# Optimization experiments

Measured on AMD Instinct MI355X. Metric: run time of the kernel, lower is better.

## Reference

```python
import jax, jax.numpy as jnp
import numpy as np

N = 100000   # nodes
E = 1600000  # edges
IN, H, C = 128, 128, 40


def setup_inputs() -> dict:
    key = jax.random.key(0)
    ks = jax.random.split(key, 8)
    feat = jax.random.normal(ks[0], (N, IN), jnp.float32)
    src = jax.random.randint(ks[1], (E,), 0, N, jnp.int32)
    dst = jax.random.randint(ks[2], (E,), 0, N, jnp.int32)
    # Glorot-ish init like dgl GraphConv.reset_parameters
    W0 = jax.random.normal(ks[3], (IN, H), jnp.float32) * (1.0 / np.sqrt(IN))
    W1 = jax.random.normal(ks[4], (H, H), jnp.float32) * (1.0 / np.sqrt(H))
    W2 = jax.random.normal(ks[5], (H, C), jnp.float32) * (1.0 / np.sqrt(H))
    b0 = jnp.zeros((H,), jnp.float32)
    b1 = jnp.zeros((H,), jnp.float32)
    b2 = jnp.zeros((C,), jnp.float32)
    return {"feat": feat, "src": src, "dst": dst,
            "W0": W0, "b0": b0, "W1": W1, "b1": b1, "W2": W2, "b2": b2}


def _graph_conv(h, src, dst, W, b):
    # dgl GraphConv with norm='both': D_out^{-1/2} pre-scale, sum-aggregate,
    # D_in^{-1/2} post-scale; degrees clamped to min 1. Weight applied before
    # aggregation (in_feats >= out_feats path) -- math is identical either way.
    ones = jnp.ones((src.shape[0],), h.dtype)
    deg_out = jnp.maximum(jax.ops.segment_sum(ones, src, num_segments=N), 1.0)
    deg_in = jnp.maximum(jax.ops.segment_sum(ones, dst, num_segments=N), 1.0)
    h = h * (deg_out ** -0.5)[:, None]
    h = h @ W                                   # [N, out]
    agg = jax.ops.segment_sum(h[src], dst, num_segments=N)  # gather+scatter
    return agg * (deg_in ** -0.5)[:, None] + b


def reference(feat, src, dst, W0, b0, W1, b1, W2, b2):
    h = jax.nn.relu(_graph_conv(feat, src, dst, W0, b0))  # dropout p=0 -> identity
    h = jax.nn.relu(_graph_conv(h, src, dst, W1, b1))
    return _graph_conv(h, src, dst, W2, b2)
```

## Files before the change

kernel.cpp:

```cpp
#include <hip/hip_runtime.h>

#define NN 100000
#define EE 1600000
#define ELLW 64
#define GEMMN ((NN + 31) / 32)
#define BQ ((EE / 4 + 511) / 512)
#define GRID_BG (BQ * 5)

#define NBKT 196
#define BSH 9
#define CAPD 10240
#define CAPS 10240

typedef int iv4 __attribute__((ext_vector_type(4)));

__device__ __forceinline__ unsigned int pack_bf2(float a, float b) {
    unsigned int ua = __float_as_uint(a);
    ua += 0x7FFFu + ((ua >> 16) & 1u);
    unsigned int ub = __float_as_uint(b);
    ub += 0x7FFFu + ((ub >> 16) & 1u);
    return (ua >> 16) | (ub & 0xFFFF0000u);
}

__device__ __forceinline__ unsigned short bf1(float a) {
    unsigned int ua = __float_as_uint(a);
    ua += 0x7FFFu + ((ua >> 16) & 1u);
    return (unsigned short)(ua >> 16);
}

__device__ __forceinline__ void gemm128_body(const float* __restrict__ X,
                                             const float* __restrict__ W, unsigned int* __restrict__ Y,
                                             int row0, int tid, float* Xs) {
    const float4* X4 = (const float4*)X;
#pragma unroll
    for (int idx = tid; idx < 1024; idx += 256) {
        int r = idx & 31, c4 = idx >> 5;
        int row = row0 + r;
        float4 v = X4[(size_t)row * 32 + c4];
        Xs[(c4 * 4 + 0) * 32 + r] = v.x;
        Xs[(c4 * 4 + 1) * 32 + r] = v.y;
        Xs[(c4 * 4 + 2) * 32 + r] = v.z;
        Xs[(c4 * 4 + 3) * 32 + r] = v.w;
    }
    __syncthreads();
    int cg = tid & 31;
    int rg = tid >> 5;
    float a[4][4];
#pragma unroll
    for (int r = 0; r < 4; ++r)
#pragma unroll
        for (int c = 0; c < 4; ++c) a[r][c] = 0.f;
    const float4* W4 = (const float4*)W;
#pragma unroll 4
    for (int k = 0; k < 128; ++k) {
        float4 xv = *(const float4*)&Xs[k * 32 + rg * 4];
        float4 wv = W4[k * 32 + cg];
        float xr[4] = {xv.x, xv.y, xv.z, xv.w};
        float wc[4] = {wv.x, wv.y, wv.z, wv.w};
#pragma unroll
        for (int r = 0; r < 4; ++r)
#pragma unroll
            for (int c = 0; c < 4; ++c) a[r][c] = fmaf(xr[r], wc[c], a[r][c]);
    }
    int rbase = row0 + rg * 4;
    uint2* Y2 = (uint2*)Y;
#pragma unroll
    for (int r = 0; r < 4; ++r) {
        Y2[(size_t)(rbase + r) * 32 + cg] =
            make_uint2(pack_bf2(a[r][0], a[r][1]), pack_bf2(a[r][2], a[r][3]));
    }
}

__global__ __launch_bounds__(256) void k_buildA_gemm0(const int* __restrict__ src, const int* __restrict__ dst,
                                                      int* __restrict__ curD, int* __restrict__ curS,
                                                      unsigned int* __restrict__ stagD,
                                                      unsigned short* __restrict__ stagS,
                                                      const float* __restrict__ X, const float* __restrict__ W,
                                                      unsigned int* __restrict__ Y) {
    __shared__ float Xs[128 * 32];
    int tid = threadIdx.x;
    int q = blockIdx.x / 5, rem = blockIdx.x % 5;
    if (rem) {
        int g = q * 4 + (rem - 1);
        if (g < GEMMN) gemm128_body(X, W, Y, g * 32, tid, Xs);
        return;
    }
    int* sh = (int*)Xs;
    for (int i = tid; i < 1536; i += 256) sh[i] = 0;
    __syncthreads();

    const iv4* s4p = (const iv4*)src;
    const iv4* d4p = (const iv4*)dst;
    const int n4 = EE / 4;
    iv4 sv[2], dv[2];
    int have[2];
#pragma unroll
    for (int h = 0; h < 2; ++h) {
        int i4 = q * 512 + h * 256 + tid;
        have[h] = (i4 < n4);
        if (have[h]) {
            sv[h] = __builtin_nontemporal_load(&s4p[i4]);
            dv[h] = __builtin_nontemporal_load(&d4p[i4]);
        }
    }
#pragma unroll
    for (int h = 0; h < 2; ++h) {
        if (have[h]) {
            int ss[4] = {sv[h].x, sv[h].y, sv[h].z, sv[h].w};
            int dd[4] = {dv[h].x, dv[h].y, dv[h].z, dv[h].w};
#pragma unroll
            for (int k = 0; k < 4; ++k) {
                atomicAdd(&sh[dd[k] >> BSH], 1);
                atomicAdd(&sh[256 + (ss[k] >> BSH)], 1);
            }
        }
    }
    __syncthreads();
    if (tid < NBKT) {
        int hd = sh[tid];
        sh[512 + tid] = hd ? atomicAdd(&curD[tid], hd) : 0;
        int hs = sh[256 + tid];
        sh[768 + tid] = hs ? atomicAdd(&curS[tid], hs) : 0;
    }
    __syncthreads();
#pragma unroll
    for (int h = 0; h < 2; ++h) {
        if (have[h]) {
            int ss[4] = {sv[h].x, sv[h].y, sv[h].z, sv[h].w};
            int dd[4] = {dv[h].x, dv[h].y, dv[h].z, dv[h].w};
#pragma unroll
            for (int k = 0; k < 4; ++k) {
                int bd = dd[k] >> BSH;
                int od = atomicAdd(&sh[1024 + bd], 1);
                stagD[(size_t)bd * CAPD + sh[512 + bd] + od] =
                    ((unsigned int)ss[k] << BSH) | (unsigned int)(dd[k] & 511);
                int bs = ss[k] >> BSH;
                int os = atomicAdd(&sh[1280 + bs], 1);
                stagS[(size_t)bs * CAPS + sh[768 + bs] + os] = (unsigned short)(ss[k] & 511);
            }
        }
    }
}

__global__ __launch_bounds__(256) void k_buildB(const int* __restrict__ curD, const int* __restrict__ curS,
                                                const unsigned int* __restrict__ stagD,
                                                const unsigned short* __restrict__ stagS,
                                                int* __restrict__ din, int* __restrict__ dout,
                                                int* __restrict__ ell) {
    __shared__ int cl[512];
    int tid = threadIdx.x;
    int b = blockIdx.x;
    for (int i = tid; i < 512; i += 256) cl[i] = 0;
    __syncthreads();
    if (b < NBKT) {
        int n0 = b << BSH;
        int cnt = min(curD[b], CAPD);
        const unsigned int* sg = stagD + (size_t)b * CAPD;
        for (int i = tid; i < cnt; i += 256) {
            unsigned int v = sg[i];
            int dlow = (int)(v & 511u);
            int s = (int)(v >> BSH);
            int p = atomicAdd(&cl[dlow], 1);
            if (p < ELLW) ell[(size_t)(n0 + dlow) * ELLW + p] = s;
        }
        __syncthreads();
        for (int i = tid; i < 512; i += 256) {
            int node = n0 + i;
            if (node < NN) din[node] = cl[i];
        }
    } else {
        int bs = b - NBKT;
        int n0 = bs << BSH;
        int cnt = min(curS[bs], CAPS);
        const unsigned short* sg = stagS + (size_t)bs * CAPS;
        for (int i = tid; i < cnt; i += 256) {
            atomicAdd(&cl[sg[i]], 1);
        }
        __syncthreads();
        for (int i = tid; i < 512; i += 256) {
            int node = n0 + i;
            if (node < NN) dout[node] = cl[i];
        }
    }
}

#define GG_BATCH(CL, SC, JB, CNT, SO) do {                                         \
    int cc_[8]; float mk_[8]; uint2 t_[8];                                         \
    _Pragma("unroll")                                                              \
    for (int k = 0; k < 8; ++k) {                                                  \
        int slot = (JB) + k;                                                       \
        int srcl = (hl << 5) | (slot & 31);                                        \
        cc_[k] = __shfl((CL), srcl);                                               \
        float sw = (SO) ? __shfl((SC), srcl) : 1.f;                                \
        mk_[k] = (slot < (CNT)) ? sw : 0.f;                                        \
    }                                                                              \
    _Pragma("unroll")                                                              \
    for (int k = 0; k < 8; ++k) {                                                  \
        t_[k] = make_uint2(0u, 0u);                                                \
        if ((JB) + k < (CNT)) t_[k] = h2v[(size_t)cc_[k] * 32 + ln];               \
    }                                                                              \
    _Pragma("unroll")                                                              \
    for (int k = 0; k < 8; ++k) {                                                  \
        a0 = fmaf(mk_[k], __uint_as_float(t_[k].x << 16), a0);                     \
        a1 = fmaf(mk_[k], __uint_as_float(t_[k].x & 0xFFFF0000u), a1);             \
        a2 = fmaf(mk_[k], __uint_as_float(t_[k].y << 16), a2);                     \
        a3 = fmaf(mk_[k], __uint_as_float(t_[k].y & 0xFFFF0000u), a3);             \
    }                                                                              \
} while (0)

__global__ __launch_bounds__(256) void k_gathergemm128(const unsigned int* __restrict__ h,
                                                       const int* __restrict__ din, const int* __restrict__ dout,
                                                       const int* __restrict__ ell,
                                                       const float* __restrict__ bias,
                                                       const float* __restrict__ W,
                                                       unsigned int* __restrict__ Y, int so_mode) {
    __shared__ float Xs[128 * 36];
    int tid = threadIdx.x;
    int wv = tid >> 6, lane = tid & 63;
    int hl = lane >> 5, ln = lane & 31;
    int row0 = blockIdx.x * 32;
    int nb = row0 + wv * 8 + hl;
    int dvh[4], dvo[4], cl0[4], cl1[4];
    float sc0[4], sc1[4];
#pragma unroll
    for (int it = 0; it < 4; ++it) {
        int v = nb + it * 2;
        dvh[it] = din[v];
        dvo[it] = dout[v];
        cl0[it] = ell[(size_t)v * ELLW + ln];
        cl1[it] = ell[(size_t)v * ELLW + 32 + ln];
    }
#pragma unroll
    for (int it = 0; it < 4; ++it) {
        int cnt = min(dvh[it], ELLW);
        int d0 = 1, d1 = 1;
        if (so_mode && ln < cnt) d0 = dout[cl0[it]];
        if (so_mode && ln + 32 < cnt) d1 = dout[cl1[it]];
        sc0[it] = rsqrtf((float)max(1, d0));
        sc1[it] = rsqrtf((float)max(1, d1));
    }
    float4 bb = ((const float4*)bias)[ln];
    const uint2* h2v = (const uint2*)h;
#pragma unroll
    for (int it = 0; it < 4; ++it) {
        int r = wv * 8 + it * 2 + hl;
        int cnt = min(dvh[it], ELLW);
        float a0 = 0.f, a1 = 0.f, a2 = 0.f, a3 = 0.f;
        for (int jb = 0; jb < 32; jb += 8) {
            if (!__any(jb < cnt)) break;
            GG_BATCH(cl0[it], sc0[it], jb, cnt, so_mode);
        }
        if (__any(cnt > 32)) {
            for (int jb = 32; jb < 64; jb += 8) {
                if (!__any(jb < cnt)) break;
                GG_BATCH(cl1[it], sc1[it], jb, cnt, so_mode);
            }
        }
        float si = rsqrtf((float)max(1, dvh[it]));
        float so = rsqrtf((float)max(1, dvo[it]));
        Xs[(4 * ln + 0) * 36 + r] = fmaxf(a0 * si + bb.x, 0.f) * so;
        Xs[(4 * ln + 1) * 36 + r] = fmaxf(a1 * si + bb.y, 0.f) * so;
        Xs[(4 * ln + 2) * 36 + r] = fmaxf(a2 * si + bb.z, 0.f) * so;
        Xs[(4 * ln + 3) * 36 + r] = fmaxf(a3 * si + bb.w, 0.f) * so;
    }
    __syncthreads();
    int cg = tid & 31, rg = tid >> 5;
    float a[4][4];
#pragma unroll
    for (int r = 0; r < 4; ++r)
#pragma unroll
        for (int c = 0; c < 4; ++c) a[r][c] = 0.f;
    const float4* W4 = (const float4*)W;
#pragma unroll 4
    for (int k = 0; k < 128; ++k) {
        float4 xv = *(const float4*)&Xs[k * 36 + rg * 4];
        float4 wv4 = W4[k * 32 + cg];
        float xr[4] = {xv.x, xv.y, xv.z, xv.w};
        float wc[4] = {wv4.x, wv4.y, wv4.z, wv4.w};
#pragma unroll
        for (int r = 0; r < 4; ++r)
#pragma unroll
            for (int c = 0; c < 4; ++c) a[r][c] = fmaf(xr[r], wc[c], a[r][c]);
    }
    int rbase = row0 + rg * 4;
    uint2* Y2 = (uint2*)Y;
#pragma unroll
    for (int r = 0; r < 4; ++r) {
        Y2[(size_t)(rbase + r) * 32 + cg] =
            make_uint2(pack_bf2(a[r][0], a[r][1]), pack_bf2(a[r][2], a[r][3]));
    }
}

__global__ __launch_bounds__(256) void k_gathergemm40(const unsigned int* __restrict__ h,
                                                      const int* __restrict__ din, const int* __restrict__ dout,
                                                      const int* __restrict__ ell,
                                                      const float* __restrict__ bias,
                                                      const float* __restrict__ W,
                                                      unsigned short* __restrict__ Y) {
    __shared__ float Xs[128 * 36];
    int tid = threadIdx.x;
    int wv = tid >> 6, lane = tid & 63;
    int hl = lane >> 5, ln = lane & 31;
    int row0 = blockIdx.x * 32;
    int nb = row0 + wv * 8 + hl;
    int dvh[4], dvo[4], cl0[4], cl1[4];
#pragma unroll
    for (int it = 0; it < 4; ++it) {
        int v = nb + it * 2;
        dvh[it] = din[v];
        dvo[it] = dout[v];
        cl0[it] = ell[(size_t)v * ELLW + ln];
        cl1[it] = ell[(size_t)v * ELLW + 32 + ln];
    }
    float4 bb = ((const float4*)bias)[ln];
    const uint2* h2v = (const uint2*)h;
#pragma unroll
    for (int it = 0; it < 4; ++it) {
        int r = wv * 8 + it * 2 + hl;
        int cnt = min(dvh[it], ELLW);
        float a0 = 0.f, a1 = 0.f, a2 = 0.f, a3 = 0.f;
        float dummy = 0.f;
        for (int jb = 0; jb < 32; jb += 8) {
            if (!__any(jb < cnt)) break;
            GG_BATCH(cl0[it], dummy, jb, cnt, 0);
        }
        if (__any(cnt > 32)) {
            for (int jb = 32; jb < 64; jb += 8) {
                if (!__any(jb < cnt)) break;
                GG_BATCH(cl1[it], dummy, jb, cnt, 0);
            }
        }
        float si = rsqrtf((float)max(1, dvh[it]));
        float so = rsqrtf((float)max(1, dvo[it]));
        Xs[(4 * ln + 0) * 36 + r] = fmaxf(a0 * si + bb.x, 0.f) * so;
        Xs[(4 * ln + 1) * 36 + r] = fmaxf(a1 * si + bb.y, 0.f) * so;
        Xs[(4 * ln + 2) * 36 + r] = fmaxf(a2 * si + bb.z, 0.f) * so;
        Xs[(4 * ln + 3) * 36 + r] = fmaxf(a3 * si + bb.w, 0.f) * so;
    }
    __syncthreads();
    int rg = tid >> 3;
    int cg = tid & 7;
    float a[5] = {0.f, 0.f, 0.f, 0.f, 0.f};
#pragma unroll 4
    for (int k = 0; k < 128; ++k) {
        float x = Xs[k * 36 + rg];
#pragma unroll
        for (int c = 0; c < 5; ++c) a[c] = fmaf(x, W[k * 40 + cg * 5 + c], a[c]);
    }
    size_t yb = (size_t)(row0 + rg) * 64 + cg * 5;
#pragma unroll
    for (int c = 0; c < 5; ++c) Y[yb + c] = bf1(a[c]);
}

__global__ __launch_bounds__(256) void k_gather40(const unsigned int* __restrict__ h, const int* __restrict__ din,
                                                  const int* __restrict__ ell,
                                                  const float* __restrict__ b, float* __restrict__ out, int n) {
    int tid = threadIdx.x;
    int wv = tid >> 6, lane = tid & 63;
    int hl = lane >> 5, ln = lane & 31;
    int v = blockIdx.x * 8 + wv * 2 + hl;
    int dv = din[v];
    int cnt = min(dv, ELLW);
    int cl0 = ell[(size_t)v * ELLW + ln];
    int cl1 = ell[(size_t)v * ELLW + 32 + ln];
    float s0 = 0.f, s1 = 0.f;
    for (int half = 0; half < 2; ++half) {
        int clh = half ? cl1 : cl0;
        int jb0 = half * 32;
        if (half && !__any(cnt > 32)) break;
        for (int jb = jb0; jb < jb0 + 32; jb += 8) {
            if (!__any(jb < cnt)) break;
            int cc_[8]; float mk_[8]; unsigned int t_[8];
#pragma unroll
            for (int k = 0; k < 8; ++k) {
                int slot = jb + k;
                int srcl = (hl << 5) | (slot & 31);
                cc_[k] = __shfl(clh, srcl);
                mk_[k] = (slot < cnt) ? 1.f : 0.f;
            }
#pragma unroll
            for (int k = 0; k < 8; ++k) {
                t_[k] = 0u;
                if (jb + k < cnt) t_[k] = h[(size_t)cc_[k] * 32 + ln];
            }
#pragma unroll
            for (int k = 0; k < 8; ++k) {
                s0 = fmaf(mk_[k], __uint_as_float(t_[k] << 16), s0);
                s1 = fmaf(mk_[k], __uint_as_float(t_[k] & 0xFFFF0000u), s1);
            }
        }
    }
    if (ln < 20) {
        float si = rsqrtf((float)max(1, dv));
        float2 bb = ((const float2*)b)[ln];
        ((float2*)out)[(size_t)v * 20 + ln] = make_float2(s0 * si + bb.x, s1 * si + bb.y);
    }
}

extern "C" void kernel_launch(void* const* d_in, const int* in_sizes, int n_in,
                              void* d_out, int out_size, void* d_ws, size_t ws_size,
                              hipStream_t stream) {
    const float* feat = (const float*)d_in[0];
    const int*   src  = (const int*)d_in[1];
    const int*   dst  = (const int*)d_in[2];
    const float* W0   = (const float*)d_in[3];
    const float* b0   = (const float*)d_in[4];
    const float* W1   = (const float*)d_in[5];
    const float* b1   = (const float*)d_in[6];
    const float* W2   = (const float*)d_in[7];
    const float* b2   = (const float*)d_in[8];
    float* out = (float*)d_out;

    char* w = (char*)d_ws;
    int*   din       = (int*)w;    w += (size_t)NN * 4;
    int*   dout      = (int*)w;    w += (size_t)NN * 4;
    int*   curD      = (int*)w;    w += 256 * 4;
    int*   curS      = (int*)w;    w += 256 * 4;
    int*   ell       = (int*)w;    w += (size_t)NN * ELLW * 4;
    unsigned int*   stagD = (unsigned int*)w;   w += (size_t)NBKT * CAPD * 4;
    unsigned short* stagS = (unsigned short*)w; w += (size_t)NBKT * CAPS * 2;
    unsigned int* h2 = (unsigned int*)w; w += (size_t)NN * 128 * 2;
    unsigned int* h2b = (unsigned int*)w; w += (size_t)NN * 128 * 2;
    unsigned int* h40 = (unsigned int*)w; w += (size_t)NN * 32 * 4;

    (void)hipMemsetAsync(d_ws, 0, (size_t)NN * 8 + 2048, stream);

    k_buildA_gemm0<<<GRID_BG, 256, 0, stream>>>(src, dst, curD, curS, stagD, stagS, feat, W0, h2);
    k_buildB<<<NBKT * 2, 256, 0, stream>>>(curD, curS, stagD, stagS, din, dout, ell);
    k_gathergemm128<<<GEMMN, 256, 0, stream>>>(h2, din, dout, ell, b0, W1, h2b, 1);
    k_gathergemm40<<<GEMMN, 256, 0, stream>>>(h2b, din, dout, ell, b1, W2, (unsigned short*)h40);
    k_gather40<<<NN / 8, 256, 0, stream>>>(h40, din, ell, b2, out, NN);
}
```

Baseline: 477.2 us.

## Split fused gather-GEMM by feature half with XCC-aware work queue and combine pass

Splits each fused gather+GEMM layer into two work items per 32-row tile, one per half of the input features. Each item gathers only 64 columns and computes a partial GEMM into fp32 scratch, and a separate combine kernel sums the two partials and packs them to bf16. Work items come from an atomic queue keyed by the XCC id so that each feature half tends to stay on the same set of dies, aiming to improve L2 locality for the gathered rows. This adds fp32 partial writes and reads plus two extra launches, falls back to the old path when the workspace is too small, and also skips loading the second ELL half when the degree is at most 32.

```diff
diff --git a/kernel.cpp b/kernel.cpp
--- a/kernel.cpp
+++ b/kernel.cpp
@@ -12,7 +12,10 @@
 #define CAPD 10240
 #define CAPS 10240
 
+#define XCC_GETREG_IMM 63508
+
 typedef int iv4 __attribute__((ext_vector_type(4)));
+typedef float fv4 __attribute__((ext_vector_type(4)));
 
 __device__ __forceinline__ unsigned int pack_bf2(float a, float b) {
     unsigned int ua = __float_as_uint(a);
@@ -35,16 +38,14 @@
 #pragma unroll
     for (int idx = tid; idx < 1024; idx += 256) {
         int r = idx & 31, c4 = idx >> 5;
-        int row = row0 + r;
-        float4 v = X4[(size_t)row * 32 + c4];
+        float4 v = X4[(size_t)(row0 + r) * 32 + c4];
         Xs[(c4 * 4 + 0) * 32 + r] = v.x;
         Xs[(c4 * 4 + 1) * 32 + r] = v.y;
         Xs[(c4 * 4 + 2) * 32 + r] = v.z;
         Xs[(c4 * 4 + 3) * 32 + r] = v.w;
     }
     __syncthreads();
-    int cg = tid & 31;
-    int rg = tid >> 5;
+    int cg = tid & 31, rg = tid >> 5;
     float a[4][4];
 #pragma unroll
     for (int r = 0; r < 4; ++r)
@@ -181,6 +182,218 @@
             int node = n0 + i;
             if (node < NN) dout[node] = cl[i];
         }
+    }
+}
+
+#define GH_BATCH(CL, SC, JB, CNT) do {                                             \
+    int cc_[8]; float mk_[8]; unsigned int t_[8];                                  \
+    _Pragma("unroll")                                                              \
+    for (int k = 0; k < 8; ++k) {                                                  \
+        int slot = (JB) + k;                                                       \
+        int srcl = (hl << 5) | (slot & 31);                                        \
+        cc_[k] = __shfl((CL), srcl);                                               \
+        float sw = so_mode ? __shfl((SC), srcl) : 1.f;                             \
+        mk_[k] = (slot < (CNT)) ? sw : 0.f;                                        \
+    }                                                                              \
+    _Pragma("unroll")                                                              \
+    for (int k = 0; k < 8; ++k) {                                                  \
+        t_[k] = 0u;                                                                \
+        if ((JB) + k < (CNT)) t_[k] = hh[(size_t)cc_[k] * 64 + ln];                \
+    }                                                                              \
+    _Pragma("unroll")                                                              \
+    for (int k = 0; k < 8; ++k) {                                                  \
+        a0 = fmaf(mk_[k], __uint_as_float(t_[k] << 16), a0);                       \
+        a1 = fmaf(mk_[k], __uint_as_float(t_[k] & 0xFFFF0000u), a1);               \
+    }                                                                              \
+} while (0)
+
+__device__ __forceinline__ int grab_item(int* q, int tid, int* sh_item) {
+    if (tid == 0) {
+        unsigned int xcc = __builtin_amdgcn_s_getreg(XCC_GETREG_IMM);
+        int g = (xcc >> 2) & 1;
+        int t = atomicAdd(&q[g], 1);
+        if (t >= GEMMN) { g ^= 1; t = atomicAdd(&q[g], 1); }
+        *sh_item = (t < GEMMN) ? (t * 2 + g) : -1;
+    }
+    __syncthreads();
+    return *sh_item;
+}
+
+__global__ __launch_bounds__(256) void k_gg128half(const unsigned int* __restrict__ h,
+                                                   const int* __restrict__ din, const int* __restrict__ dout,
+                                                   const int* __restrict__ ell,
+                                                   const float* __restrict__ bias,
+                                                   const float* __restrict__ W,
+                                                   float* __restrict__ P, int* __restrict__ q,
+                                                   int so_mode) {
+    __shared__ float Xs[64 * 36];
+    __shared__ int sh_item;
+    int tid = threadIdx.x;
+    int item = grab_item(q, tid, &sh_item);
+    if (item < 0) return;
+    int tile = item >> 1, half = item & 1;
+    int wv = tid >> 6, lane = tid & 63, hl = lane >> 5, ln = lane & 31;
+    int row0 = tile * 32;
+    int nb = row0 + wv * 8 + hl;
+    int dvh[4], dvo[4], cl0[4], cl1[4];
+    float sc0[4], sc1[4];
+#pragma unroll
+    for (int it = 0; it < 4; ++it) {
+        int v = nb + it * 2;
+        dvh[it] = din[v];
+        dvo[it] = dout[v];
+        cl0[it] = ell[(size_t)v * ELLW + ln];
+        cl1[it] = (dvh[it] > 32) ? ell[(size_t)v * ELLW + 32 + ln] : 0;
+    }
+#pragma unroll
+    for (int it = 0; it < 4; ++it) {
+        int cnt = min(dvh[it], ELLW);
+        int d0 = 1, d1 = 1;
+        if (so_mode && ln < cnt) d0 = dout[cl0[it]];
+        if (so_mode && ln + 32 < cnt) d1 = dout[cl1[it]];
+        sc0[it] = rsqrtf((float)max(1, d0));
+        sc1[it] = rsqrtf((float)max(1, d1));
+    }
+    float2 bb = ((const float2*)bias)[32 * half + ln];
+    const unsigned int* hh = h + 32 * half;
+#pragma unroll
+    for (int it = 0; it < 4; ++it) {
+        int r = wv * 8 + it * 2 + hl;
+        int cnt = min(dvh[it], ELLW);
+        float a0 = 0.f, a1 = 0.f;
+        for (int jb = 0; jb < 32; jb += 8) {
+            if (!__any(jb < cnt)) break;
+            GH_BATCH(cl0[it], sc0[it], jb, cnt);
+        }
+        if (__any(cnt > 32)) {
+            for (int jb = 32; jb < 64; jb += 8) {
+                if (!__any(jb < cnt)) break;
+                GH_BATCH(cl1[it], sc1[it], jb, cnt);
+            }
+        }
+        float si = rsqrtf((float)max(1, dvh[it]));
+        float so = rsqrtf((float)max(1, dvo[it]));
+        Xs[(2 * ln + 0) * 36 + r] = fmaxf(a0 * si + bb.x, 0.f) * so;
+        Xs[(2 * ln + 1) * 36 + r] = fmaxf(a1 * si + bb.y, 0.f) * so;
+    }
+    __syncthreads();
+    int cg = tid & 31, rg = tid >> 5;
+    float a[4][4];
+#pragma unroll
+    for (int r = 0; r < 4; ++r)
+#pragma unroll
+        for (int c = 0; c < 4; ++c) a[r][c] = 0.f;
+    const float4* W4 = (const float4*)W;
+    int kbase = 64 * half;
+#pragma unroll 4
+    for (int k = 0; k < 64; ++k) {
+        float4 xv = *(const float4*)&Xs[k * 36 + rg * 4];
+        float4 wv4 = W4[(kbase + k) * 32 + cg];
+        float xr[4] = {xv.x, xv.y, xv.z, xv.w};
+        float wc[4] = {wv4.x, wv4.y, wv4.z, wv4.w};
+#pragma unroll
+        for (int r = 0; r < 4; ++r)
+#pragma unroll
+            for (int c = 0; c < 4; ++c) a[r][c] = fmaf(xr[r], wc[c], a[r][c]);
+    }
+    float* Pp = P + (size_t)half * NN * 128;
+    int rbase = row0 + rg * 4;
+#pragma unroll
+    for (int r = 0; r < 4; ++r) {
+        fv4 vv = {a[r][0], a[r][1], a[r][2], a[r][3]};
+        __builtin_nontemporal_store(vv, (fv4*)&Pp[(size_t)(rbase + r) * 128 + cg * 4]);
+    }
+}
+
+__global__ __launch_bounds__(256) void k_combine128(const float* __restrict__ P,
+                                                    unsigned int* __restrict__ Y) {
+    const fv4* P0 = (const fv4*)P;
+    const fv4* P1 = (const fv4*)(P + (size_t)NN * 128);
+    int total = NN * 32;
+    for (int i = blockIdx.x * 256 + threadIdx.x; i < total; i += gridDim.x * 256) {
+        fv4 u = __builtin_nontemporal_load(&P0[i]);
+        fv4 v = __builtin_nontemporal_load(&P1[i]);
+        ((uint2*)Y)[i] = make_uint2(pack_bf2(u.x + v.x, u.y + v.y),
+                                    pack_bf2(u.z + v.z, u.w + v.w));
+    }
+}
+
+__global__ __launch_bounds__(256) void k_gg40half(const unsigned int* __restrict__ h,
+                                                  const int* __restrict__ din, const int* __restrict__ dout,
+                                                  const int* __restrict__ ell,
+                                                  const float* __restrict__ bias,
+                                                  const float* __restrict__ W,
+                                                  float* __restrict__ P, int* __restrict__ q) {
+    __shared__ float Xs[64 * 36];
+    __shared__ int sh_item;
+    const int so_mode = 0;
+    int tid = threadIdx.x;
+    int item = grab_item(q, tid, &sh_item);
+    if (item < 0) return;
+    int tile = item >> 1, half = item & 1;
+    int wv = tid >> 6, lane = tid & 63, hl = lane >> 5, ln = lane & 31;
+    int row0 = tile * 32;
+    int nb = row0 + wv * 8 + hl;
+    int dvh[4], dvo[4], cl0[4], cl1[4];
+#pragma unroll
+    for (int it = 0; it < 4; ++it) {
+        int v = nb + it * 2;
+        dvh[it] = din[v];
+        dvo[it] = dout[v];
+        cl0[it] = ell[(size_t)v * ELLW + ln];
+        cl1[it] = (dvh[it] > 32) ? ell[(size_t)v * ELLW + 32 + ln] : 0;
+    }
+    float2 bb = ((const float2*)bias)[32 * half + ln];
+    const unsigned int* hh = h + 32 * half;
+#pragma unroll
+    for (int it = 0; it < 4; ++it) {
+        int r = wv * 8 + it * 2 + hl;
+        int cnt = min(dvh[it], ELLW);
+        float a0 = 0.f, a1 = 0.f;
+        float dummy = 0.f;
+        for (int jb = 0; jb < 32; jb += 8) {
+            if (!__any(jb < cnt)) break;
+            GH_BATCH(cl0[it], dummy, jb, cnt);
+        }
+        if (__any(cnt > 32)) {
+            for (int jb = 32; jb < 64; jb += 8) {
+                if (!__any(jb < cnt)) break;
+                GH_BATCH(cl1[it], dummy, jb, cnt);
+            }
+        }
+        float si = rsqrtf((float)max(1, dvh[it]));
+        float so = rsqrtf((float)max(1, dvo[it]));
+        Xs[(2 * ln + 0) * 36 + r] = fmaxf(a0 * si + bb.x, 0.f) * so;
+        Xs[(2 * ln + 1) * 36 + r] = fmaxf(a1 * si + bb.y, 0.f) * so;
+    }
+    __syncthreads();
+    int rg = tid >> 3;
+    int cg = tid & 7;
+    float a[5] = {0.f, 0.f, 0.f, 0.f, 0.f};
+    int kbase = 64 * half;
+#pragma unroll 4
+    for (int k = 0; k < 64; ++k) {
+        float x = Xs[k * 36 + rg];
+#pragma unroll
+        for (int c = 0; c < 5; ++c) a[c] = fmaf(x, W[(kbase + k) * 40 + cg * 5 + c], a[c]);
+    }
+    float* Pp = P + (size_t)half * NN * 40 + (size_t)(row0 + rg) * 40 + cg * 5;
+#pragma unroll
+    for (int c = 0; c < 5; ++c) __builtin_nontemporal_store(a[c], &Pp[c]);
+}
+
+__global__ __launch_bounds__(256) void k_combine40(const float* __restrict__ P,
+                                                   unsigned int* __restrict__ Y) {
+    const float* P0 = P;
+    const float* P1 = P + (size_t)NN * 40;
+    int total = NN * 20;
+    for (int i = blockIdx.x * 256 + threadIdx.x; i < total; i += gridDim.x * 256) {
+        int node = i / 20, c = i - node * 20;
+        float s0 = __builtin_nontemporal_load(&P0[node * 40 + 2 * c]) +
+                   __builtin_nontemporal_load(&P1[node * 40 + 2 * c]);
+        float s1 = __builtin_nontemporal_load(&P0[node * 40 + 2 * c + 1]) +
+                   __builtin_nontemporal_load(&P1[node * 40 + 2 * c + 1]);
+        Y[(size_t)node * 32 + c] = pack_bf2(s0, s1);
     }
 }
 
@@ -362,7 +575,7 @@
     int dv = din[v];
     int cnt = min(dv, ELLW);
     int cl0 = ell[(size_t)v * ELLW + ln];
-    int cl1 = ell[(size_t)v * ELLW + 32 + ln];
+    int cl1 = (dv > 32) ? ell[(size_t)v * ELLW + 32 + ln] : 0;
     float s0 = 0.f, s1 = 0.f;
     for (int half = 0; half < 2; ++half) {
         int clh = half ? cl1 : cl0;
@@ -412,22 +625,47 @@
     float* out = (float*)d_out;
 
     char* w = (char*)d_ws;
-    int*   din       = (int*)w;    w += (size_t)NN * 4;
-    int*   dout      = (int*)w;    w += (size_t)NN * 4;
-    int*   curD      = (int*)w;    w += 256 * 4;
-    int*   curS      = (int*)w;    w += 256 * 4;
-    int*   ell       = (int*)w;    w += (size_t)NN * ELLW * 4;
-    unsigned int*   stagD = (unsigned int*)w;   w += (size_t)NBKT * CAPD * 4;
-    unsigned short* stagS = (unsigned short*)w; w += (size_t)NBKT * CAPS * 2;
-    unsigned int* h2 = (unsigned int*)w; w += (size_t)NN * 128 * 2;
-    unsigned int* h2b = (unsigned int*)w; w += (size_t)NN * 128 * 2;
-    unsigned int* h40 = (unsigned int*)w; w += (size_t)NN * 32 * 4;
-
-    (void)hipMemsetAsync(d_ws, 0, (size_t)NN * 8 + 2048, stream);
-
-    k_buildA_gemm0<<<GRID_BG, 256, 0, stream>>>(src, dst, curD, curS, stagD, stagS, feat, W0, h2);
-    k_buildB<<<NBKT * 2, 256, 0, stream>>>(curD, curS, stagD, stagS, din, dout, ell);
-    k_gathergemm128<<<GEMMN, 256, 0, stream>>>(h2, din, dout, ell, b0, W1, h2b, 1);
-    k_gathergemm40<<<GEMMN, 256, 0, stream>>>(h2b, din, dout, ell, b1, W2, (unsigned short*)h40);
-    k_gather40<<<NN / 8, 256, 0, stream>>>(h40, din, ell, b2, out, NN);
-}
+    int*   din  = (int*)w;  w += (size_t)NN * 4;
+    int*   dout = (int*)w;  w += (size_t)NN * 4;
+    int*   curD = (int*)w;  w += 1024;
+    int*   curS = (int*)w;  w += 1024;
+    int*   qq   = (int*)w;  w += 2048;
+    int*   ell  = (int*)w;  w += (size_t)NN * ELLW * 4;
+
+    const size_t A_SZ = (size_t)NN * 128 * 4 * 2;
+    const size_t HDR = (size_t)NN * 8 + 4096;
+    const size_t NEED_NEW = HDR + (size_t)NN * ELLW * 4 + A_SZ +
+                            (size_t)NN * 128 * 2 + (size_t)NN * 32 * 4;
+
+    (void)hipMemsetAsync(d_ws, 0, HDR, stream);
+
+    if (ws_size >= NEED_NEW) {
+        char* A = w;  w += A_SZ;
+        unsigned int*   stagD = (unsigned int*)A;
+        unsigned short* stagS = (unsigned short*)(A + (size_t)NBKT * CAPD * 4);
+        float* P   = (float*)A;
+        float* P40 = (float*)A;
+        unsigned int* hB  = (unsigned int*)w; w += (size_t)NN * 128 * 2;
+        unsigned int* h40 = (unsigned int*)w;
+
+        k_buildA_gemm0<<<GRID_BG, 256, 0, stream>>>(src, dst, curD, curS, stagD, stagS, feat, W0, hB);
+        k_buildB<<<NBKT * 2, 256, 0, stream>>>(curD, curS, stagD, stagS, din, dout, ell);
+        k_gg128half<<<GEMMN * 2, 256, 0, stream>>>(hB, din, dout, ell, b0, W1, P, qq, 1);
+        k_combine128<<<2048, 256, 0, stream>>>(P, hB);
+        k_gg40half<<<GEMMN * 2, 256, 0, stream>>>(hB, din, dout, ell, b1, W2, P40, qq + 2);
+        k_combine40<<<1024, 256, 0, stream>>>(P40, h40);
+        k_gather40<<<NN / 8, 256, 0, stream>>>(h40, din, ell, b2, out, NN);
+    } else {
+        unsigned int*   stagD = (unsigned int*)w;   w += (size_t)NBKT * CAPD * 4;
+        unsigned short* stagS = (unsigned short*)w; w += (size_t)NBKT * CAPS * 2;
+        unsigned int* h2  = (unsigned int*)w; w += (size_t)NN * 128 * 2;
+        unsigned int* h2b = (unsigned int*)w; w += (size_t)NN * 128 * 2;
+        unsigned int* h40 = (unsigned int*)w;
+
+        k_buildA_gemm0<<<GRID_BG, 256, 0, stream>>>(src, dst, curD, curS, stagD, stagS, feat, W0, h2);
+        k_buildB<<<NBKT * 2, 256, 0, stream>>>(curD, curS, stagD, stagS, din, dout, ell);
+        k_gathergemm128<<<GEMMN, 256, 0, stream>>>(h2, din, dout, ell, b0, W1, h2b, 1);
+        k_gathergemm40<<<GEMMN, 256, 0, stream>>>(h2b, din, dout, ell, b1, W2, (unsigned short*)h40);
+        k_gather40<<<NN / 8, 256, 0, stream>>>(h40, din, ell, b2, out, NN);
+    }
+}
```

Result: slower. 587.1 us (+23.0%).
